# Performance work log

Hardware: AMD Instinct MI355X
Metric: run time of the kernel (lower is better)

The kernel has to match this reference:

```python
import jax, jax.numpy as jnp
import numpy as np

B, T, D, HD = 8, 2048, 768, 64

def setup_inputs() -> dict:
    key = jax.random.key(0)
    k1, k2, k3, k4 = jax.random.split(key, 4)
    scale = 1.0 / np.sqrt(D)
    return {
        "x": jax.random.normal(k1, (B, T, D), dtype=jnp.float32),
        "Wq": jax.random.normal(k2, (D, HD), dtype=jnp.float32) * scale,
        "Wk": jax.random.normal(k3, (D, HD), dtype=jnp.float32) * scale,
        "Wv": jax.random.normal(k4, (D, HD), dtype=jnp.float32) * scale,
    }

def reference(x, Wq, Wk, Wv):
    # q,k,v: [B,T,HD]
    q = jnp.einsum('btd,dh->bth', x, Wq)
    k = jnp.einsum('btd,dh->bth', x, Wk)
    v = jnp.einsum('btd,dh->bth', x, Wv)
    dk = q.shape[-1]
    # scores: [B,T,T], scaled then causally masked with -inf
    scores = jnp.einsum('bqh,bkh->bqk', q, k) / jnp.sqrt(jnp.float32(dk))
    Tq = scores.shape[-1]
    causal = jnp.tril(jnp.ones((Tq, Tq), dtype=bool))
    scores = jnp.where(causal, scores, -jnp.inf)
    attn = jax.nn.softmax(scores, axis=-1)  # dropout rate 0 (eval mode)
    return jnp.einsum('bqk,bkh->bqh', attn, v)
```

## Files before the change

### kernel.cpp

```cpp
#include <hip/hip_runtime.h>
#include <hip/hip_bf16.h>
#include <stdint.h>

#define B_  8
#define T_  2048
#define D_  768
#define HD_ 64
#define M_  (B_ * T_)

typedef short s16x8 __attribute__((ext_vector_type(8)));
typedef float f32x4 __attribute__((ext_vector_type(4)));
typedef float f32x16 __attribute__((ext_vector_type(16)));
typedef unsigned int u32;

union Frag { uint4 u; s16x8 h; };

__device__ __forceinline__ unsigned short f2bf(float f) {
    unsigned u = __builtin_bit_cast(unsigned, f);
    u += 0x7FFFu + ((u >> 16) & 1u);
    return (unsigned short)(u >> 16);
}
__device__ __forceinline__ unsigned pack_bf16x2(float lo, float hi) {
    return (unsigned)f2bf(lo) | ((unsigned)f2bf(hi) << 16);
}
__device__ __forceinline__ unsigned cvt_pk(float lo, float hi) {
    unsigned r;
    asm("v_cvt_pk_bf16_f32 %0, %1, %2" : "=v"(r) : "v"(lo), "v"(hi));
    return r;
}

__device__ __forceinline__ void gl_lds16(const void* g, void* l) {
    __builtin_amdgcn_global_load_lds(
        (const __attribute__((address_space(1))) u32*)g,
        (__attribute__((address_space(3))) u32*)l, 16, 0, 0);
}

__global__ __launch_bounds__(64) void prep_pk(const float* __restrict__ Wq,
                                              const float* __restrict__ Wk,
                                              const float* __restrict__ Wv,
                                              unsigned short* __restrict__ pk) {
    int nb = blockIdx.x / 24, kk = blockIdx.x % 24;
    int lane = threadIdx.x, g = lane >> 4, t = lane & 15;
    int mat = nb >> 2, col = (nb & 3) * 16 + t;
    const float* W = (mat == 0) ? Wq : (mat == 1) ? Wk : Wv;
    float s = (mat == 0) ? 0.18033688011112042f : 1.0f;
    float v[8];
#pragma unroll
    for (int e = 0; e < 8; e++)
        v[e] = W[(size_t)(kk * 32 + g * 8 + e) * HD_ + col] * s;
    uint4 u;
    u.x = pack_bf16x2(v[0], v[1]);
    u.y = pack_bf16x2(v[2], v[3]);
    u.z = pack_bf16x2(v[4], v[5]);
    u.w = pack_bf16x2(v[6], v[7]);
    *(uint4*)(pk + ((size_t)blockIdx.x * 64 + lane) * 8) = u;
}

__global__ __launch_bounds__(256, 2) void qkv_proj(const float* __restrict__ x,
                                                   const unsigned short* __restrict__ pk,
                                                   unsigned short* __restrict__ qo,
                                                   unsigned short* __restrict__ ko,
                                                   unsigned short* __restrict__ vt) {
    __shared__ char xs[4][8192];

    int tid = threadIdx.x, w = tid >> 6, lane = tid & 63;
    int g = lane >> 4, t = lane & 15;
    int m0 = blockIdx.x * 32;

    auto STAGE = [&](int jb) {
        int buf = jb & 3;
#pragma unroll
        for (int h = 0; h < 2; h++) {
            int s = tid + h * 256;
            int row = s >> 4;
            int a = (s & 15) ^ (row & 15);
            gl_lds16(x + (size_t)(m0 + row) * D_ + jb * 64 + a * 4,
                     &xs[buf][(w * 64 + h * 256) * 16]);
        }
    };

    const unsigned short* wp = pk + (size_t)w * 36864;
    auto LOADB = [&](Frag (&bb)[6], int jb) {
#pragma unroll
        for (int j = 0; j < 3; j++)
#pragma unroll
            for (int c = 0; c < 2; c++)
                bb[j * 2 + c].u = *(const uint4*)(wp + ((size_t)(j * 24 + jb * 2 + c) * 64 + lane) * 8);
    };

    f32x4 acc[3][2];
#pragma unroll
    for (int j = 0; j < 3; j++)
#pragma unroll
        for (int mf = 0; mf < 2; mf++) acc[j][mf] = (f32x4){0.f, 0.f, 0.f, 0.f};

    Frag bfr[3][6];
    LOADB(bfr[0], 0);
    LOADB(bfr[1], 1);
    STAGE(0); STAGE(1); STAGE(2);

#pragma unroll
    for (int jb = 0; jb < 12; jb++) {
        if (jb + 2 < 12) LOADB(bfr[(jb + 2) % 3], jb + 2);
        if (jb == 0)       asm volatile("s_waitcnt vmcnt(10)" ::: "memory");
        else if (jb == 10) asm volatile("s_waitcnt vmcnt(8)"  ::: "memory");
        else if (jb == 11) asm volatile("s_waitcnt vmcnt(0)"  ::: "memory");
        else               asm volatile("s_waitcnt vmcnt(16)" ::: "memory");
        __builtin_amdgcn_s_barrier();
        if (jb + 3 < 12) STAGE(jb + 3);
        int buf = jb & 3;

        Frag af[2][2];
#pragma unroll
        for (int mf = 0; mf < 2; mf++) {
            int r32 = mf * 16 + t;
#pragma unroll
            for (int c = 0; c < 2; c++) {
                float4 f0 = *(const float4*)(&xs[buf][r32 * 256 + (((c * 8 + g * 2 + 0) ^ t) * 16)]);
                float4 f1 = *(const float4*)(&xs[buf][r32 * 256 + (((c * 8 + g * 2 + 1) ^ t) * 16)]);
                af[mf][c].u.x = cvt_pk(f0.x, f0.y);
                af[mf][c].u.y = cvt_pk(f0.z, f0.w);
                af[mf][c].u.z = cvt_pk(f1.x, f1.y);
                af[mf][c].u.w = cvt_pk(f1.z, f1.w);
            }
        }
        __builtin_amdgcn_s_setprio(1);
#pragma unroll
        for (int j = 0; j < 3; j++)
#pragma unroll
            for (int c = 0; c < 2; c++) {
                acc[j][0] = __builtin_amdgcn_mfma_f32_16x16x32_bf16(af[0][c].h, bfr[jb % 3][j * 2 + c].h, acc[j][0], 0, 0, 0);
                acc[j][1] = __builtin_amdgcn_mfma_f32_16x16x32_bf16(af[1][c].h, bfr[jb % 3][j * 2 + c].h, acc[j][1], 0, 0, 0);
            }
        __builtin_amdgcn_s_setprio(0);
    }

#pragma unroll
    for (int j = 0; j < 3; j++) {
        int nb = w * 3 + j;
        int col = (nb & 3) * 16 + t;
#pragma unroll
        for (int mf = 0; mf < 2; mf++) {
            int row0 = m0 + mf * 16;
            if (nb < 8) {
                unsigned short* dst = (nb < 4) ? qo : ko;
#pragma unroll
                for (int r = 0; r < 4; r++)
                    dst[(size_t)(row0 + g * 4 + r) * HD_ + col] = f2bf(acc[j][mf][r]);
            } else {
                int bb = m0 >> 11;
                int trow = (row0 & 2047) + g * 4;
                uint2 pkk;
                pkk.x = cvt_pk(acc[j][mf][0], acc[j][mf][1]);
                pkk.y = cvt_pk(acc[j][mf][2], acc[j][mf][3]);
                *(uint2*)(vt + (((size_t)(bb * HD_ + col)) << 11) + trow) = pkk;
            }
        }
    }
}

__global__ __launch_bounds__(256) void attn(const unsigned short* __restrict__ qw,
                                            const unsigned short* __restrict__ kw,
                                            const unsigned short* __restrict__ vt,
                                            float* __restrict__ out) {
    __shared__ char smem[65536];

    int tid = threadIdx.x, wv = tid >> 6, lane = tid & 63;
    int hi = lane >> 5, l31 = lane & 31;
    int blk = blockIdx.x;
    int b = blk & 7, idx = blk >> 3;
    int qblk = (idx < 32) ? (63 - idx) : (idx - 32);
    int q0 = qblk * 32;
    int qg = q0 + l31;
    size_t bbase = (size_t)b * T_;
    int nt = qblk + 1;
    int ks = wv;
    int mt = (nt > ks) ? ((nt - ks + 3) >> 2) : 0;

    const unsigned short* kp = kw + bbase * HD_;
    const unsigned short* vp = vt + ((size_t)(b * HD_) << 11);
    char* KV = smem + wv * 16384;

    Frag qf[4];
#pragma unroll
    for (int c = 0; c < 4; c++)
        qf[c].u = *(const uint4*)(qw + (bbase + qg) * HD_ + c * 16 + hi * 8);

    auto STAGE = [&](int j, int buf) {
        int jj = (j < nt) ? j : (nt - 1);
        int kv0 = jj * 32;
#pragma unroll
        for (int q = 0; q < 4; q++) {
            int kr = q * 8 + (lane >> 3);
            int ka = (lane & 7) ^ (kr & 7);
            gl_lds16(kp + (size_t)(kv0 + kr) * HD_ + ka * 8, KV + buf * 4096 + q * 1024);
        }
#pragma unroll
        for (int q = 0; q < 4; q++) {
            int vd = q * 16 + (lane >> 2);
            int va = (lane & 3) ^ (vd & 3) ^ ((vd >> 2) & 3);
            gl_lds16(vp + ((size_t)vd << 11) + kv0 + va * 8, KV + 8192 + buf * 4096 + q * 1024);
        }
    };

    f32x16 o0, o1;
#pragma unroll
    for (int r = 0; r < 16; r++) { o0[r] = 0.f; o1[r] = 0.f; }
    float lacc = 0.f;

    auto QK = [&](const char* KB, f32x16& st) {
#pragma unroll
        for (int r = 0; r < 16; r++) st[r] = 0.f;
        __builtin_amdgcn_s_setprio(1);
#pragma unroll
        for (int c = 0; c < 4; c++) {
            Frag ka;
            ka.u = *(const uint4*)(KB + l31 * 128 + (((c * 2 + hi) ^ (l31 & 7)) * 16));
            st = __builtin_amdgcn_mfma_f32_32x32x16_bf16(ka.h, qf[c].h, st, 0, 0, 0);
        }
        __builtin_amdgcn_s_setprio(0);
    };

    auto SMPV = [&](f32x16& st, int j, const char* VB) {
        int kv0 = j * 32;
        if (j == qblk) {
#pragma unroll
            for (int r = 0; r < 16; r++) {
                int key = kv0 + (r & 3) + 8 * (r >> 2) + 4 * hi;
                if (key > qg) st[r] = -1e30f;
            }
        }
        float p[16], ss = 0.f;
#pragma unroll
        for (int r = 0; r < 16; r++) { p[r] = exp2f(st[r]); ss += p[r]; }
        lacc += ss;

        u32 A0 = cvt_pk(p[0], p[1]),   A1 = cvt_pk(p[2], p[3]);
        u32 B0 = cvt_pk(p[4], p[5]),   B1 = cvt_pk(p[6], p[7]);
        u32 C0 = cvt_pk(p[8], p[9]),   C1 = cvt_pk(p[10], p[11]);
        u32 D0 = cvt_pk(p[12], p[13]), D1 = cvt_pk(p[14], p[15]);
        u32 A0x = (u32)__shfl_xor((int)A0, 32);
        u32 A1x = (u32)__shfl_xor((int)A1, 32);
        u32 B0x = (u32)__shfl_xor((int)B0, 32);
        u32 B1x = (u32)__shfl_xor((int)B1, 32);
        u32 C0x = (u32)__shfl_xor((int)C0, 32);
        u32 C1x = (u32)__shfl_xor((int)C1, 32);
        u32 D0x = (u32)__shfl_xor((int)D0, 32);
        u32 D1x = (u32)__shfl_xor((int)D1, 32);
        Frag pf0, pf1;
        pf0.u.x = hi ? B0x : A0;
        pf0.u.y = hi ? B1x : A1;
        pf0.u.z = hi ? B0  : A0x;
        pf0.u.w = hi ? B1  : A1x;
        pf1.u.x = hi ? D0x : C0;
        pf1.u.y = hi ? D1x : C1;
        pf1.u.z = hi ? D0  : C0x;
        pf1.u.w = hi ? D1  : C1x;

        __builtin_amdgcn_s_setprio(1);
        {
            int sw0 = (l31 & 3) ^ ((l31 >> 2) & 3);
            Frag va;
            va.u = *(const uint4*)(VB + l31 * 64 + (((hi) ^ sw0) * 16));
            o0 = __builtin_amdgcn_mfma_f32_32x32x16_bf16(va.h, pf0.h, o0, 0, 0, 0);
            va.u = *(const uint4*)(VB + l31 * 64 + (((2 + hi) ^ sw0) * 16));
            o0 = __builtin_amdgcn_mfma_f32_32x32x16_bf16(va.h, pf1.h, o0, 0, 0, 0);
            int d1 = 32 + l31;
            int sw1 = (d1 & 3) ^ ((d1 >> 2) & 3);
            va.u = *(const uint4*)(VB + d1 * 64 + (((hi) ^ sw1) * 16));
            o1 = __builtin_amdgcn_mfma_f32_32x32x16_bf16(va.h, pf0.h, o1, 0, 0, 0);
            va.u = *(const uint4*)(VB + d1 * 64 + (((2 + hi) ^ sw1) * 16));
            o1 = __builtin_amdgcn_mfma_f32_32x32x16_bf16(va.h, pf1.h, o1, 0, 0, 0);
        }
        __builtin_amdgcn_s_setprio(0);
    };

    if (mt > 0) STAGE(ks, 0);
    if (mt > 1) STAGE(ks + 4, 1);

    int i = 0;
#pragma unroll 1
    for (; i + 2 <= mt; i += 2) {
        int ja = ks + 4 * i, jb2 = ja + 4;
        const char* KA = KV + (i & 1) * 4096;
        const char* VA = KV + 8192 + (i & 1) * 4096;
        const char* KB2 = KV + ((i + 1) & 1) * 4096;
        const char* VB2 = KV + 8192 + ((i + 1) & 1) * 4096;

        asm volatile("s_waitcnt vmcnt(12)" ::: "memory");
        f32x16 sa;
        QK(KA, sa);
        asm volatile("s_waitcnt vmcnt(4)" ::: "memory");
        f32x16 sb;
        QK(KB2, sb);
        SMPV(sa, ja, VA);
        asm volatile("s_waitcnt vmcnt(0)" ::: "memory");
        if (i + 2 < mt) STAGE(ks + 4 * (i + 2), i & 1);
        SMPV(sb, jb2, VB2);
        if (i + 3 < mt) STAGE(ks + 4 * (i + 3), (i + 1) & 1);
    }
    if (i < mt) {
        int ja = ks + 4 * i;
        const char* KA = KV + (i & 1) * 4096;
        const char* VA = KV + 8192 + (i & 1) * 4096;
        asm volatile("s_waitcnt vmcnt(4)" ::: "memory");
        f32x16 sa;
        QK(KA, sa);
        asm volatile("s_waitcnt vmcnt(0)" ::: "memory");
        SMPV(sa, ja, VA);
    }

    asm volatile("s_waitcnt vmcnt(0)" ::: "memory");
    lacc += __shfl_xor(lacc, 32);
    __syncthreads();

    float* MO = (float*)smem;
    {
        int base = (wv * 64 + lane) * 36;
#pragma unroll
        for (int qd = 0; qd < 4; qd++) {
            float4 w4;
            w4.x = o0[qd * 4 + 0]; w4.y = o0[qd * 4 + 1];
            w4.z = o0[qd * 4 + 2]; w4.w = o0[qd * 4 + 3];
            *(float4*)&MO[base + qd * 4] = w4;
            float4 v4;
            v4.x = o1[qd * 4 + 0]; v4.y = o1[qd * 4 + 1];
            v4.z = o1[qd * 4 + 2]; v4.w = o1[qd * 4 + 3];
            *(float4*)&MO[base + 16 + qd * 4] = v4;
        }
        MO[base + 32] = lacc;
    }
    __syncthreads();
    {
        int row = tid >> 3;
        int c0 = (tid & 7) * 8;
        int j0 = 4 * ((c0 & 31) >> 3) + ((c0 >> 5) << 4);
        float lsum = 0.f;
#pragma unroll
        for (int k = 0; k < 4; k++) lsum += MO[(k * 64 + row) * 36 + 32];
        float inv = 1.0f / lsum;
        float4 aq = {0.f, 0.f, 0.f, 0.f};
        float4 bq = {0.f, 0.f, 0.f, 0.f};
#pragma unroll
        for (int k = 0; k < 4; k++) {
            float4 v0 = *(const float4*)&MO[(k * 64 + row) * 36 + j0];
            float4 v1 = *(const float4*)&MO[(k * 64 + row + 32) * 36 + j0];
            aq.x += v0.x; aq.y += v0.y; aq.z += v0.z; aq.w += v0.w;
            bq.x += v1.x; bq.y += v1.y; bq.z += v1.z; bq.w += v1.w;
        }
        aq.x *= inv; aq.y *= inv; aq.z *= inv; aq.w *= inv;
        bq.x *= inv; bq.y *= inv; bq.z *= inv; bq.w *= inv;
        float* op = out + (bbase + q0 + row) * HD_ + c0;
        *(float4*)&op[0] = aq;
        *(float4*)&op[4] = bq;
    }
}

extern "C" void kernel_launch(void* const* d_in, const int* in_sizes, int n_in,
                              void* d_out, int out_size, void* d_ws, size_t ws_size,
                              hipStream_t stream) {
    const float* x  = (const float*)d_in[0];
    const float* Wq = (const float*)d_in[1];
    const float* Wk = (const float*)d_in[2];
    const float* Wv = (const float*)d_in[3];
    char* ws = (char*)d_ws;
    unsigned short* pkw = (unsigned short*)ws;
    unsigned short* qw = (unsigned short*)(ws + 294912);
    unsigned short* kw = (unsigned short*)(ws + 294912 + 2097152);
    unsigned short* vt = (unsigned short*)(ws + 294912 + 4194304);
    float* out = (float*)d_out;

    hipLaunchKernelGGL(prep_pk, dim3(288), dim3(64), 0, stream, Wq, Wk, Wv, pkw);
    hipLaunchKernelGGL(qkv_proj, dim3(M_ / 32), dim3(256), 0, stream, x, pkw, qw, kw, vt);
    hipLaunchKernelGGL(attn, dim3(512), dim3(256), 0, stream, qw, kw, vt, out);
}
```

Baseline: 41.99 us.

## Fuse weight packing, QKV projection and attention into one persistent kernel

Merges the three launches (weight pack, QKV projection, causal attention) into a single kernel of 512 blocks. The phases are separated by software grid barriers built on an atomic counter in the workspace, which is zeroed by a memset before each launch. The goal is to remove launch gaps and the tail drain between kernels. In exchange it adds a memset, two global spin barriers, and a deadlock risk unless all 512 blocks are resident at once. Using launch bounds of 2 blocks per SM with 64KB of LDS also means the attention phase runs at the occupancy set for the projection.

```diff
diff --git a/kernel.cpp b/kernel.cpp
--- a/kernel.cpp
+++ b/kernel.cpp
@@ -7,6 +7,7 @@
 #define D_  768
 #define HD_ 64
 #define M_  (B_ * T_)
+#define NBLK 512
 
 typedef short s16x8 __attribute__((ext_vector_type(8)));
 typedef float f32x4 __attribute__((ext_vector_type(4)));
@@ -35,324 +36,343 @@
         (__attribute__((address_space(3))) u32*)l, 16, 0, 0);
 }
 
-__global__ __launch_bounds__(64) void prep_pk(const float* __restrict__ Wq,
-                                              const float* __restrict__ Wk,
-                                              const float* __restrict__ Wv,
-                                              unsigned short* __restrict__ pk) {
-    int nb = blockIdx.x / 24, kk = blockIdx.x % 24;
-    int lane = threadIdx.x, g = lane >> 4, t = lane & 15;
-    int mat = nb >> 2, col = (nb & 3) * 16 + t;
-    const float* W = (mat == 0) ? Wq : (mat == 1) ? Wk : Wv;
-    float s = (mat == 0) ? 0.18033688011112042f : 1.0f;
-    float v[8];
-#pragma unroll
-    for (int e = 0; e < 8; e++)
-        v[e] = W[(size_t)(kk * 32 + g * 8 + e) * HD_ + col] * s;
-    uint4 u;
-    u.x = pack_bf16x2(v[0], v[1]);
-    u.y = pack_bf16x2(v[2], v[3]);
-    u.z = pack_bf16x2(v[4], v[5]);
-    u.w = pack_bf16x2(v[6], v[7]);
-    *(uint4*)(pk + ((size_t)blockIdx.x * 64 + lane) * 8) = u;
-}
-
-__global__ __launch_bounds__(256, 2) void qkv_proj(const float* __restrict__ x,
-                                                   const unsigned short* __restrict__ pk,
-                                                   unsigned short* __restrict__ qo,
-                                                   unsigned short* __restrict__ ko,
-                                                   unsigned short* __restrict__ vt) {
-    __shared__ char xs[4][8192];
-
-    int tid = threadIdx.x, w = tid >> 6, lane = tid & 63;
-    int g = lane >> 4, t = lane & 15;
-    int m0 = blockIdx.x * 32;
-
-    auto STAGE = [&](int jb) {
-        int buf = jb & 3;
-#pragma unroll
-        for (int h = 0; h < 2; h++) {
-            int s = tid + h * 256;
-            int row = s >> 4;
-            int a = (s & 15) ^ (row & 15);
-            gl_lds16(x + (size_t)(m0 + row) * D_ + jb * 64 + a * 4,
-                     &xs[buf][(w * 64 + h * 256) * 16]);
-        }
-    };
-
-    const unsigned short* wp = pk + (size_t)w * 36864;
-    auto LOADB = [&](Frag (&bb)[6], int jb) {
-#pragma unroll
-        for (int j = 0; j < 3; j++)
-#pragma unroll
-            for (int c = 0; c < 2; c++)
-                bb[j * 2 + c].u = *(const uint4*)(wp + ((size_t)(j * 24 + jb * 2 + c) * 64 + lane) * 8);
-    };
-
-    f32x4 acc[3][2];
-#pragma unroll
-    for (int j = 0; j < 3; j++)
-#pragma unroll
-        for (int mf = 0; mf < 2; mf++) acc[j][mf] = (f32x4){0.f, 0.f, 0.f, 0.f};
-
-    Frag bfr[3][6];
-    LOADB(bfr[0], 0);
-    LOADB(bfr[1], 1);
-    STAGE(0); STAGE(1); STAGE(2);
-
-#pragma unroll
-    for (int jb = 0; jb < 12; jb++) {
-        if (jb + 2 < 12) LOADB(bfr[(jb + 2) % 3], jb + 2);
-        if (jb == 0)       asm volatile("s_waitcnt vmcnt(10)" ::: "memory");
-        else if (jb == 10) asm volatile("s_waitcnt vmcnt(8)"  ::: "memory");
-        else if (jb == 11) asm volatile("s_waitcnt vmcnt(0)"  ::: "memory");
-        else               asm volatile("s_waitcnt vmcnt(16)" ::: "memory");
-        __builtin_amdgcn_s_barrier();
-        if (jb + 3 < 12) STAGE(jb + 3);
-        int buf = jb & 3;
-
-        Frag af[2][2];
-#pragma unroll
-        for (int mf = 0; mf < 2; mf++) {
-            int r32 = mf * 16 + t;
-#pragma unroll
-            for (int c = 0; c < 2; c++) {
-                float4 f0 = *(const float4*)(&xs[buf][r32 * 256 + (((c * 8 + g * 2 + 0) ^ t) * 16)]);
-                float4 f1 = *(const float4*)(&xs[buf][r32 * 256 + (((c * 8 + g * 2 + 1) ^ t) * 16)]);
-                af[mf][c].u.x = cvt_pk(f0.x, f0.y);
-                af[mf][c].u.y = cvt_pk(f0.z, f0.w);
-                af[mf][c].u.z = cvt_pk(f1.x, f1.y);
-                af[mf][c].u.w = cvt_pk(f1.z, f1.w);
-            }
-        }
-        __builtin_amdgcn_s_setprio(1);
-#pragma unroll
-        for (int j = 0; j < 3; j++)
-#pragma unroll
-            for (int c = 0; c < 2; c++) {
-                acc[j][0] = __builtin_amdgcn_mfma_f32_16x16x32_bf16(af[0][c].h, bfr[jb % 3][j * 2 + c].h, acc[j][0], 0, 0, 0);
-                acc[j][1] = __builtin_amdgcn_mfma_f32_16x16x32_bf16(af[1][c].h, bfr[jb % 3][j * 2 + c].h, acc[j][1], 0, 0, 0);
-            }
-        __builtin_amdgcn_s_setprio(0);
-    }
-
-#pragma unroll
-    for (int j = 0; j < 3; j++) {
-        int nb = w * 3 + j;
-        int col = (nb & 3) * 16 + t;
-#pragma unroll
-        for (int mf = 0; mf < 2; mf++) {
-            int row0 = m0 + mf * 16;
-            if (nb < 8) {
-                unsigned short* dst = (nb < 4) ? qo : ko;
-#pragma unroll
-                for (int r = 0; r < 4; r++)
-                    dst[(size_t)(row0 + g * 4 + r) * HD_ + col] = f2bf(acc[j][mf][r]);
-            } else {
-                int bb = m0 >> 11;
-                int trow = (row0 & 2047) + g * 4;
-                uint2 pkk;
-                pkk.x = cvt_pk(acc[j][mf][0], acc[j][mf][1]);
-                pkk.y = cvt_pk(acc[j][mf][2], acc[j][mf][3]);
-                *(uint2*)(vt + (((size_t)(bb * HD_ + col)) << 11) + trow) = pkk;
-            }
-        }
-    }
-}
-
-__global__ __launch_bounds__(256) void attn(const unsigned short* __restrict__ qw,
-                                            const unsigned short* __restrict__ kw,
-                                            const unsigned short* __restrict__ vt,
-                                            float* __restrict__ out) {
-    __shared__ char smem[65536];
-
-    int tid = threadIdx.x, wv = tid >> 6, lane = tid & 63;
-    int hi = lane >> 5, l31 = lane & 31;
-    int blk = blockIdx.x;
-    int b = blk & 7, idx = blk >> 3;
-    int qblk = (idx < 32) ? (63 - idx) : (idx - 32);
-    int q0 = qblk * 32;
-    int qg = q0 + l31;
-    size_t bbase = (size_t)b * T_;
-    int nt = qblk + 1;
-    int ks = wv;
-    int mt = (nt > ks) ? ((nt - ks + 3) >> 2) : 0;
-
-    const unsigned short* kp = kw + bbase * HD_;
-    const unsigned short* vp = vt + ((size_t)(b * HD_) << 11);
-    char* KV = smem + wv * 16384;
-
-    Frag qf[4];
-#pragma unroll
-    for (int c = 0; c < 4; c++)
-        qf[c].u = *(const uint4*)(qw + (bbase + qg) * HD_ + c * 16 + hi * 8);
-
-    auto STAGE = [&](int j, int buf) {
-        int jj = (j < nt) ? j : (nt - 1);
-        int kv0 = jj * 32;
-#pragma unroll
-        for (int q = 0; q < 4; q++) {
-            int kr = q * 8 + (lane >> 3);
-            int ka = (lane & 7) ^ (kr & 7);
-            gl_lds16(kp + (size_t)(kv0 + kr) * HD_ + ka * 8, KV + buf * 4096 + q * 1024);
-        }
-#pragma unroll
-        for (int q = 0; q < 4; q++) {
-            int vd = q * 16 + (lane >> 2);
-            int va = (lane & 3) ^ (vd & 3) ^ ((vd >> 2) & 3);
-            gl_lds16(vp + ((size_t)vd << 11) + kv0 + va * 8, KV + 8192 + buf * 4096 + q * 1024);
-        }
-    };
-
-    f32x16 o0, o1;
-#pragma unroll
-    for (int r = 0; r < 16; r++) { o0[r] = 0.f; o1[r] = 0.f; }
-    float lacc = 0.f;
-
-    auto QK = [&](const char* KB, f32x16& st) {
-#pragma unroll
-        for (int r = 0; r < 16; r++) st[r] = 0.f;
-        __builtin_amdgcn_s_setprio(1);
-#pragma unroll
-        for (int c = 0; c < 4; c++) {
-            Frag ka;
-            ka.u = *(const uint4*)(KB + l31 * 128 + (((c * 2 + hi) ^ (l31 & 7)) * 16));
-            st = __builtin_amdgcn_mfma_f32_32x32x16_bf16(ka.h, qf[c].h, st, 0, 0, 0);
-        }
-        __builtin_amdgcn_s_setprio(0);
-    };
-
-    auto SMPV = [&](f32x16& st, int j, const char* VB) {
-        int kv0 = j * 32;
-        if (j == qblk) {
-#pragma unroll
-            for (int r = 0; r < 16; r++) {
-                int key = kv0 + (r & 3) + 8 * (r >> 2) + 4 * hi;
-                if (key > qg) st[r] = -1e30f;
-            }
-        }
-        float p[16], ss = 0.f;
-#pragma unroll
-        for (int r = 0; r < 16; r++) { p[r] = exp2f(st[r]); ss += p[r]; }
-        lacc += ss;
-
-        u32 A0 = cvt_pk(p[0], p[1]),   A1 = cvt_pk(p[2], p[3]);
-        u32 B0 = cvt_pk(p[4], p[5]),   B1 = cvt_pk(p[6], p[7]);
-        u32 C0 = cvt_pk(p[8], p[9]),   C1 = cvt_pk(p[10], p[11]);
-        u32 D0 = cvt_pk(p[12], p[13]), D1 = cvt_pk(p[14], p[15]);
-        u32 A0x = (u32)__shfl_xor((int)A0, 32);
-        u32 A1x = (u32)__shfl_xor((int)A1, 32);
-        u32 B0x = (u32)__shfl_xor((int)B0, 32);
-        u32 B1x = (u32)__shfl_xor((int)B1, 32);
-        u32 C0x = (u32)__shfl_xor((int)C0, 32);
-        u32 C1x = (u32)__shfl_xor((int)C1, 32);
-        u32 D0x = (u32)__shfl_xor((int)D0, 32);
-        u32 D1x = (u32)__shfl_xor((int)D1, 32);
-        Frag pf0, pf1;
-        pf0.u.x = hi ? B0x : A0;
-        pf0.u.y = hi ? B1x : A1;
-        pf0.u.z = hi ? B0  : A0x;
-        pf0.u.w = hi ? B1  : A1x;
-        pf1.u.x = hi ? D0x : C0;
-        pf1.u.y = hi ? D1x : C1;
-        pf1.u.z = hi ? D0  : C0x;
-        pf1.u.w = hi ? D1  : C1x;
-
-        __builtin_amdgcn_s_setprio(1);
-        {
-            int sw0 = (l31 & 3) ^ ((l31 >> 2) & 3);
-            Frag va;
-            va.u = *(const uint4*)(VB + l31 * 64 + (((hi) ^ sw0) * 16));
-            o0 = __builtin_amdgcn_mfma_f32_32x32x16_bf16(va.h, pf0.h, o0, 0, 0, 0);
-            va.u = *(const uint4*)(VB + l31 * 64 + (((2 + hi) ^ sw0) * 16));
-            o0 = __builtin_amdgcn_mfma_f32_32x32x16_bf16(va.h, pf1.h, o0, 0, 0, 0);
-            int d1 = 32 + l31;
-            int sw1 = (d1 & 3) ^ ((d1 >> 2) & 3);
-            va.u = *(const uint4*)(VB + d1 * 64 + (((hi) ^ sw1) * 16));
-            o1 = __builtin_amdgcn_mfma_f32_32x32x16_bf16(va.h, pf0.h, o1, 0, 0, 0);
-            va.u = *(const uint4*)(VB + d1 * 64 + (((2 + hi) ^ sw1) * 16));
-            o1 = __builtin_amdgcn_mfma_f32_32x32x16_bf16(va.h, pf1.h, o1, 0, 0, 0);
-        }
-        __builtin_amdgcn_s_setprio(0);
-    };
-
-    if (mt > 0) STAGE(ks, 0);
-    if (mt > 1) STAGE(ks + 4, 1);
-
-    int i = 0;
-#pragma unroll 1
-    for (; i + 2 <= mt; i += 2) {
-        int ja = ks + 4 * i, jb2 = ja + 4;
-        const char* KA = KV + (i & 1) * 4096;
-        const char* VA = KV + 8192 + (i & 1) * 4096;
-        const char* KB2 = KV + ((i + 1) & 1) * 4096;
-        const char* VB2 = KV + 8192 + ((i + 1) & 1) * 4096;
-
-        asm volatile("s_waitcnt vmcnt(12)" ::: "memory");
-        f32x16 sa;
-        QK(KA, sa);
-        asm volatile("s_waitcnt vmcnt(4)" ::: "memory");
-        f32x16 sb;
-        QK(KB2, sb);
-        SMPV(sa, ja, VA);
-        asm volatile("s_waitcnt vmcnt(0)" ::: "memory");
-        if (i + 2 < mt) STAGE(ks + 4 * (i + 2), i & 1);
-        SMPV(sb, jb2, VB2);
-        if (i + 3 < mt) STAGE(ks + 4 * (i + 3), (i + 1) & 1);
-    }
-    if (i < mt) {
-        int ja = ks + 4 * i;
-        const char* KA = KV + (i & 1) * 4096;
-        const char* VA = KV + 8192 + (i & 1) * 4096;
-        asm volatile("s_waitcnt vmcnt(4)" ::: "memory");
-        f32x16 sa;
-        QK(KA, sa);
-        asm volatile("s_waitcnt vmcnt(0)" ::: "memory");
-        SMPV(sa, ja, VA);
-    }
-
-    asm volatile("s_waitcnt vmcnt(0)" ::: "memory");
-    lacc += __shfl_xor(lacc, 32);
+__device__ __forceinline__ void grid_barrier(unsigned* cnt) {
     __syncthreads();
-
-    float* MO = (float*)smem;
-    {
-        int base = (wv * 64 + lane) * 36;
-#pragma unroll
-        for (int qd = 0; qd < 4; qd++) {
-            float4 w4;
-            w4.x = o0[qd * 4 + 0]; w4.y = o0[qd * 4 + 1];
-            w4.z = o0[qd * 4 + 2]; w4.w = o0[qd * 4 + 3];
-            *(float4*)&MO[base + qd * 4] = w4;
-            float4 v4;
-            v4.x = o1[qd * 4 + 0]; v4.y = o1[qd * 4 + 1];
-            v4.z = o1[qd * 4 + 2]; v4.w = o1[qd * 4 + 3];
-            *(float4*)&MO[base + 16 + qd * 4] = v4;
-        }
-        MO[base + 32] = lacc;
+    if (threadIdx.x == 0) {
+        __threadfence();
+        __hip_atomic_fetch_add(cnt, 1u, __ATOMIC_ACQ_REL, __HIP_MEMORY_SCOPE_AGENT);
+        while (__hip_atomic_load(cnt, __ATOMIC_ACQUIRE, __HIP_MEMORY_SCOPE_AGENT) < (unsigned)NBLK)
+            __builtin_amdgcn_s_sleep(2);
+        __threadfence();
     }
     __syncthreads();
+}
+
+__global__ __launch_bounds__(256, 2) void fused(const float* __restrict__ x,
+                                                const float* __restrict__ Wq,
+                                                const float* __restrict__ Wk,
+                                                const float* __restrict__ Wv,
+                                                unsigned short* __restrict__ pk,
+                                                unsigned short* __restrict__ qo,
+                                                unsigned short* __restrict__ ko,
+                                                unsigned short* __restrict__ vt,
+                                                float* __restrict__ out,
+                                                unsigned* __restrict__ cnt) {
+    __shared__ char smem[65536];
+    int tid = threadIdx.x, blk = blockIdx.x;
+
     {
-        int row = tid >> 3;
-        int c0 = (tid & 7) * 8;
-        int j0 = 4 * ((c0 & 31) >> 3) + ((c0 >> 5) << 4);
-        float lsum = 0.f;
-#pragma unroll
-        for (int k = 0; k < 4; k++) lsum += MO[(k * 64 + row) * 36 + 32];
-        float inv = 1.0f / lsum;
-        float4 aq = {0.f, 0.f, 0.f, 0.f};
-        float4 bq = {0.f, 0.f, 0.f, 0.f};
-#pragma unroll
-        for (int k = 0; k < 4; k++) {
-            float4 v0 = *(const float4*)&MO[(k * 64 + row) * 36 + j0];
-            float4 v1 = *(const float4*)&MO[(k * 64 + row + 32) * 36 + j0];
-            aq.x += v0.x; aq.y += v0.y; aq.z += v0.z; aq.w += v0.w;
-            bq.x += v1.x; bq.y += v1.y; bq.z += v1.z; bq.w += v1.w;
-        }
-        aq.x *= inv; aq.y *= inv; aq.z *= inv; aq.w *= inv;
-        bq.x *= inv; bq.y *= inv; bq.z *= inv; bq.w *= inv;
-        float* op = out + (bbase + q0 + row) * HD_ + c0;
-        *(float4*)&op[0] = aq;
-        *(float4*)&op[4] = bq;
+        int id = blk * 256 + tid;
+        if (id < 288 * 64) {
+            int tile = id >> 6, lane = id & 63;
+            int nb = tile / 24, kk = tile % 24;
+            int g = lane >> 4, t = lane & 15;
+            int mat = nb >> 2, col = (nb & 3) * 16 + t;
+            const float* W = (mat == 0) ? Wq : (mat == 1) ? Wk : Wv;
+            float s = (mat == 0) ? 0.18033688011112042f : 1.0f;
+            float v[8];
+#pragma unroll
+            for (int e = 0; e < 8; e++)
+                v[e] = W[(size_t)(kk * 32 + g * 8 + e) * HD_ + col] * s;
+            uint4 u;
+            u.x = pack_bf16x2(v[0], v[1]);
+            u.y = pack_bf16x2(v[2], v[3]);
+            u.z = pack_bf16x2(v[4], v[5]);
+            u.w = pack_bf16x2(v[6], v[7]);
+            *(uint4*)(pk + ((size_t)tile * 64 + lane) * 8) = u;
+        }
+    }
+    grid_barrier(cnt);
+
+    {
+        char (*xs)[8192] = (char(*)[8192])smem;
+
+        int w = tid >> 6, lane = tid & 63;
+        int g = lane >> 4, t = lane & 15;
+        int m0 = blk * 32;
+
+        auto STAGE = [&](int jb) {
+            int buf = jb & 3;
+#pragma unroll
+            for (int h = 0; h < 2; h++) {
+                int s = tid + h * 256;
+                int row = s >> 4;
+                int a = (s & 15) ^ (row & 15);
+                gl_lds16(x + (size_t)(m0 + row) * D_ + jb * 64 + a * 4,
+                         &xs[buf][(w * 64 + h * 256) * 16]);
+            }
+        };
+
+        const unsigned short* wp = pk + (size_t)w * 36864;
+        auto LOADB = [&](Frag (&bb)[6], int jb) {
+#pragma unroll
+            for (int j = 0; j < 3; j++)
+#pragma unroll
+                for (int c = 0; c < 2; c++)
+                    bb[j * 2 + c].u = *(const uint4*)(wp + ((size_t)(j * 24 + jb * 2 + c) * 64 + lane) * 8);
+        };
+
+        f32x4 acc[3][2];
+#pragma unroll
+        for (int j = 0; j < 3; j++)
+#pragma unroll
+            for (int mf = 0; mf < 2; mf++) acc[j][mf] = (f32x4){0.f, 0.f, 0.f, 0.f};
+
+        Frag bfr[3][6];
+        LOADB(bfr[0], 0);
+        LOADB(bfr[1], 1);
+        STAGE(0); STAGE(1); STAGE(2);
+
+#pragma unroll
+        for (int jb = 0; jb < 12; jb++) {
+            if (jb + 2 < 12) LOADB(bfr[(jb + 2) % 3], jb + 2);
+            if (jb == 0)       asm volatile("s_waitcnt vmcnt(10)" ::: "memory");
+            else if (jb == 10) asm volatile("s_waitcnt vmcnt(8)"  ::: "memory");
+            else if (jb == 11) asm volatile("s_waitcnt vmcnt(0)"  ::: "memory");
+            else               asm volatile("s_waitcnt vmcnt(16)" ::: "memory");
+            __builtin_amdgcn_s_barrier();
+            if (jb + 3 < 12) STAGE(jb + 3);
+            int buf = jb & 3;
+
+            Frag af[2][2];
+#pragma unroll
+            for (int mf = 0; mf < 2; mf++) {
+                int r32 = mf * 16 + t;
+#pragma unroll
+                for (int c = 0; c < 2; c++) {
+                    float4 f0 = *(const float4*)(&xs[buf][r32 * 256 + (((c * 8 + g * 2 + 0) ^ t) * 16)]);
+                    float4 f1 = *(const float4*)(&xs[buf][r32 * 256 + (((c * 8 + g * 2 + 1) ^ t) * 16)]);
+                    af[mf][c].u.x = cvt_pk(f0.x, f0.y);
+                    af[mf][c].u.y = cvt_pk(f0.z, f0.w);
+                    af[mf][c].u.z = cvt_pk(f1.x, f1.y);
+                    af[mf][c].u.w = cvt_pk(f1.z, f1.w);
+                }
+            }
+            __builtin_amdgcn_s_setprio(1);
+#pragma unroll
+            for (int j = 0; j < 3; j++)
+#pragma unroll
+                for (int c = 0; c < 2; c++) {
+                    acc[j][0] = __builtin_amdgcn_mfma_f32_16x16x32_bf16(af[0][c].h, bfr[jb % 3][j * 2 + c].h, acc[j][0], 0, 0, 0);
+                    acc[j][1] = __builtin_amdgcn_mfma_f32_16x16x32_bf16(af[1][c].h, bfr[jb % 3][j * 2 + c].h, acc[j][1], 0, 0, 0);
+                }
+            __builtin_amdgcn_s_setprio(0);
+        }
+
+#pragma unroll
+        for (int j = 0; j < 3; j++) {
+            int nb = w * 3 + j;
+            int col = (nb & 3) * 16 + t;
+#pragma unroll
+            for (int mf = 0; mf < 2; mf++) {
+                int row0 = m0 + mf * 16;
+                if (nb < 8) {
+                    unsigned short* dst = (nb < 4) ? qo : ko;
+#pragma unroll
+                    for (int r = 0; r < 4; r++)
+                        dst[(size_t)(row0 + g * 4 + r) * HD_ + col] = f2bf(acc[j][mf][r]);
+                } else {
+                    int bb = m0 >> 11;
+                    int trow = (row0 & 2047) + g * 4;
+                    uint2 pkk;
+                    pkk.x = cvt_pk(acc[j][mf][0], acc[j][mf][1]);
+                    pkk.y = cvt_pk(acc[j][mf][2], acc[j][mf][3]);
+                    *(uint2*)(vt + (((size_t)(bb * HD_ + col)) << 11) + trow) = pkk;
+                }
+            }
+        }
+    }
+    grid_barrier(cnt + 16);
+
+    {
+        int wv = tid >> 6, lane = tid & 63;
+        int hi = lane >> 5, l31 = lane & 31;
+        int b = blk & 7, idx = blk >> 3;
+        int qblk = (idx < 32) ? (63 - idx) : (idx - 32);
+        int q0 = qblk * 32;
+        int qg = q0 + l31;
+        size_t bbase = (size_t)b * T_;
+        int nt = qblk + 1;
+        int ks = wv;
+        int mt = (nt > ks) ? ((nt - ks + 3) >> 2) : 0;
+
+        const unsigned short* kp = ko + bbase * HD_;
+        const unsigned short* vp = vt + ((size_t)(b * HD_) << 11);
+        char* KV = smem + wv * 16384;
+
+        Frag qf[4];
+#pragma unroll
+        for (int c = 0; c < 4; c++)
+            qf[c].u = *(const uint4*)(qo + (bbase + qg) * HD_ + c * 16 + hi * 8);
+
+        auto STAGE = [&](int j, int buf) {
+            int jj = (j < nt) ? j : (nt - 1);
+            int kv0 = jj * 32;
+#pragma unroll
+            for (int q = 0; q < 4; q++) {
+                int kr = q * 8 + (lane >> 3);
+                int ka = (lane & 7) ^ (kr & 7);
+                gl_lds16(kp + (size_t)(kv0 + kr) * HD_ + ka * 8, KV + buf * 4096 + q * 1024);
+            }
+#pragma unroll
+            for (int q = 0; q < 4; q++) {
+                int vd = q * 16 + (lane >> 2);
+                int va = (lane & 3) ^ (vd & 3) ^ ((vd >> 2) & 3);
+                gl_lds16(vp + ((size_t)vd << 11) + kv0 + va * 8, KV + 8192 + buf * 4096 + q * 1024);
+            }
+        };
+
+        f32x16 o0, o1;
+#pragma unroll
+        for (int r = 0; r < 16; r++) { o0[r] = 0.f; o1[r] = 0.f; }
+        float lacc = 0.f;
+
+        auto QK = [&](const char* KB, f32x16& st) {
+#pragma unroll
+            for (int r = 0; r < 16; r++) st[r] = 0.f;
+            __builtin_amdgcn_s_setprio(1);
+#pragma unroll
+            for (int c = 0; c < 4; c++) {
+                Frag ka;
+                ka.u = *(const uint4*)(KB + l31 * 128 + (((c * 2 + hi) ^ (l31 & 7)) * 16));
+                st = __builtin_amdgcn_mfma_f32_32x32x16_bf16(ka.h, qf[c].h, st, 0, 0, 0);
+            }
+            __builtin_amdgcn_s_setprio(0);
+        };
+
+        auto SMPV = [&](f32x16& st, int j, const char* VB) {
+            int kv0 = j * 32;
+            if (j == qblk) {
+#pragma unroll
+                for (int r = 0; r < 16; r++) {
+                    int key = kv0 + (r & 3) + 8 * (r >> 2) + 4 * hi;
+                    if (key > qg) st[r] = -1e30f;
+                }
+            }
+            float p[16], ss = 0.f;
+#pragma unroll
+            for (int r = 0; r < 16; r++) { p[r] = exp2f(st[r]); ss += p[r]; }
+            lacc += ss;
+
+            u32 A0 = cvt_pk(p[0], p[1]),   A1 = cvt_pk(p[2], p[3]);
+            u32 B0 = cvt_pk(p[4], p[5]),   B1 = cvt_pk(p[6], p[7]);
+            u32 C0 = cvt_pk(p[8], p[9]),   C1 = cvt_pk(p[10], p[11]);
+            u32 D0 = cvt_pk(p[12], p[13]), D1 = cvt_pk(p[14], p[15]);
+            u32 A0x = (u32)__shfl_xor((int)A0, 32);
+            u32 A1x = (u32)__shfl_xor((int)A1, 32);
+            u32 B0x = (u32)__shfl_xor((int)B0, 32);
+            u32 B1x = (u32)__shfl_xor((int)B1, 32);
+            u32 C0x = (u32)__shfl_xor((int)C0, 32);
+            u32 C1x = (u32)__shfl_xor((int)C1, 32);
+            u32 D0x = (u32)__shfl_xor((int)D0, 32);
+            u32 D1x = (u32)__shfl_xor((int)D1, 32);
+            Frag pf0, pf1;
+            pf0.u.x = hi ? B0x : A0;
+            pf0.u.y = hi ? B1x : A1;
+            pf0.u.z = hi ? B0  : A0x;
+            pf0.u.w = hi ? B1  : A1x;
+            pf1.u.x = hi ? D0x : C0;
+            pf1.u.y = hi ? D1x : C1;
+            pf1.u.z = hi ? D0  : C0x;
+            pf1.u.w = hi ? D1  : C1x;
+
+            __builtin_amdgcn_s_setprio(1);
+            {
+                int sw0 = (l31 & 3) ^ ((l31 >> 2) & 3);
+                Frag va;
+                va.u = *(const uint4*)(VB + l31 * 64 + (((hi) ^ sw0) * 16));
+                o0 = __builtin_amdgcn_mfma_f32_32x32x16_bf16(va.h, pf0.h, o0, 0, 0, 0);
+                va.u = *(const uint4*)(VB + l31 * 64 + (((2 + hi) ^ sw0) * 16));
+                o0 = __builtin_amdgcn_mfma_f32_32x32x16_bf16(va.h, pf1.h, o0, 0, 0, 0);
+                int d1 = 32 + l31;
+                int sw1 = (d1 & 3) ^ ((d1 >> 2) & 3);
+                va.u = *(const uint4*)(VB + d1 * 64 + (((hi) ^ sw1) * 16));
+                o1 = __builtin_amdgcn_mfma_f32_32x32x16_bf16(va.h, pf0.h, o1, 0, 0, 0);
+                va.u = *(const uint4*)(VB + d1 * 64 + (((2 + hi) ^ sw1) * 16));
+                o1 = __builtin_amdgcn_mfma_f32_32x32x16_bf16(va.h, pf1.h, o1, 0, 0, 0);
+            }
+            __builtin_amdgcn_s_setprio(0);
+        };
+
+        if (mt > 0) STAGE(ks, 0);
+        if (mt > 1) STAGE(ks + 4, 1);
+
+        int i = 0;
+#pragma unroll 1
+        for (; i + 2 <= mt; i += 2) {
+            int ja = ks + 4 * i, jb2 = ja + 4;
+            const char* KA = KV + (i & 1) * 4096;
+            const char* VA = KV + 8192 + (i & 1) * 4096;
+            const char* KB2 = KV + ((i + 1) & 1) * 4096;
+            const char* VB2 = KV + 8192 + ((i + 1) & 1) * 4096;
+
+            asm volatile("s_waitcnt vmcnt(12)" ::: "memory");
+            f32x16 sa;
+            QK(KA, sa);
+            asm volatile("s_waitcnt vmcnt(4)" ::: "memory");
+            f32x16 sb;
+            QK(KB2, sb);
+            SMPV(sa, ja, VA);
+            asm volatile("s_waitcnt vmcnt(0)" ::: "memory");
+            if (i + 2 < mt) STAGE(ks + 4 * (i + 2), i & 1);
+            SMPV(sb, jb2, VB2);
+            if (i + 3 < mt) STAGE(ks + 4 * (i + 3), (i + 1) & 1);
+        }
+        if (i < mt) {
+            int ja = ks + 4 * i;
+            const char* KA = KV + (i & 1) * 4096;
+            const char* VA = KV + 8192 + (i & 1) * 4096;
+            asm volatile("s_waitcnt vmcnt(4)" ::: "memory");
+            f32x16 sa;
+            QK(KA, sa);
+            asm volatile("s_waitcnt vmcnt(0)" ::: "memory");
+            SMPV(sa, ja, VA);
+        }
+
+        asm volatile("s_waitcnt vmcnt(0)" ::: "memory");
+        lacc += __shfl_xor(lacc, 32);
+        __syncthreads();
+
+        float* MO = (float*)smem;
+        {
+            int base = (wv * 64 + lane) * 36;
+#pragma unroll
+            for (int qd = 0; qd < 4; qd++) {
+                float4 w4;
+                w4.x = o0[qd * 4 + 0]; w4.y = o0[qd * 4 + 1];
+                w4.z = o0[qd * 4 + 2]; w4.w = o0[qd * 4 + 3];
+                *(float4*)&MO[base + qd * 4] = w4;
+                float4 v4;
+                v4.x = o1[qd * 4 + 0]; v4.y = o1[qd * 4 + 1];
+                v4.z = o1[qd * 4 + 2]; v4.w = o1[qd * 4 + 3];
+                *(float4*)&MO[base + 16 + qd * 4] = v4;
+            }
+            MO[base + 32] = lacc;
+        }
+        __syncthreads();
+        {
+            int row = tid >> 3;
+            int c0 = (tid & 7) * 8;
+            int j0 = 4 * ((c0 & 31) >> 3) + ((c0 >> 5) << 4);
+            float lsum = 0.f;
+#pragma unroll
+            for (int k = 0; k < 4; k++) lsum += MO[(k * 64 + row) * 36 + 32];
+            float inv = 1.0f / lsum;
+            float4 aq = {0.f, 0.f, 0.f, 0.f};
+            float4 bq = {0.f, 0.f, 0.f, 0.f};
+#pragma unroll
+            for (int k = 0; k < 4; k++) {
+                float4 v0 = *(const float4*)&MO[(k * 64 + row) * 36 + j0];
+                float4 v1 = *(const float4*)&MO[(k * 64 + row + 32) * 36 + j0];
+                aq.x += v0.x; aq.y += v0.y; aq.z += v0.z; aq.w += v0.w;
+                bq.x += v1.x; bq.y += v1.y; bq.z += v1.z; bq.w += v1.w;
+            }
+            aq.x *= inv; aq.y *= inv; aq.z *= inv; aq.w *= inv;
+            bq.x *= inv; bq.y *= inv; bq.z *= inv; bq.w *= inv;
+            float* op = out + (bbase + q0 + row) * HD_ + c0;
+            *(float4*)&op[0] = aq;
+            *(float4*)&op[4] = bq;
+        }
     }
 }
 
@@ -368,9 +388,10 @@
     unsigned short* qw = (unsigned short*)(ws + 294912);
     unsigned short* kw = (unsigned short*)(ws + 294912 + 2097152);
     unsigned short* vt = (unsigned short*)(ws + 294912 + 4194304);
+    unsigned* cnt = (unsigned*)(ws + 294912 + 6291456);
     float* out = (float*)d_out;
 
-    hipLaunchKernelGGL(prep_pk, dim3(288), dim3(64), 0, stream, Wq, Wk, Wv, pkw);
-    hipLaunchKernelGGL(qkv_proj, dim3(M_ / 32), dim3(256), 0, stream, x, pkw, qw, kw, vt);
-    hipLaunchKernelGGL(attn, dim3(512), dim3(256), 0, stream, qw, kw, vt, out);
-}
+    hipMemsetAsync(cnt, 0, 128, stream);
+    hipLaunchKernelGGL(fused, dim3(NBLK), dim3(256), 0, stream,
+                       x, Wq, Wk, Wv, pkw, qw, kw, vt, out, cnt);
+}
```

After: 157.8 us. 3.76x slower.

## Fuse weight packing into projection kernel with global atomic counter handoff

Applied to the files above, without the earlier changes.

Removes the separate prep_pk launch by having the first 72 blocks of qkv_proj pack the bf16 weight fragments, then signal completion through an agent-scope atomic counter. All blocks issue their x staging loads first, spin-wait on the counter, then load the packed weights. The waitcnt values are adjusted for the reordered loads. This saves a kernel launch and its gap but adds a memset, a grid-wide spin dependency that needs the producer blocks to be resident, and extra latency for blocks waiting on the packing.

```diff
diff --git a/kernel.cpp b/kernel.cpp
--- a/kernel.cpp
+++ b/kernel.cpp
@@ -35,37 +35,45 @@
         (__attribute__((address_space(3))) u32*)l, 16, 0, 0);
 }
 
-__global__ __launch_bounds__(64) void prep_pk(const float* __restrict__ Wq,
-                                              const float* __restrict__ Wk,
-                                              const float* __restrict__ Wv,
-                                              unsigned short* __restrict__ pk) {
-    int nb = blockIdx.x / 24, kk = blockIdx.x % 24;
-    int lane = threadIdx.x, g = lane >> 4, t = lane & 15;
-    int mat = nb >> 2, col = (nb & 3) * 16 + t;
-    const float* W = (mat == 0) ? Wq : (mat == 1) ? Wk : Wv;
-    float s = (mat == 0) ? 0.18033688011112042f : 1.0f;
-    float v[8];
-#pragma unroll
-    for (int e = 0; e < 8; e++)
-        v[e] = W[(size_t)(kk * 32 + g * 8 + e) * HD_ + col] * s;
-    uint4 u;
-    u.x = pack_bf16x2(v[0], v[1]);
-    u.y = pack_bf16x2(v[2], v[3]);
-    u.z = pack_bf16x2(v[4], v[5]);
-    u.w = pack_bf16x2(v[6], v[7]);
-    *(uint4*)(pk + ((size_t)blockIdx.x * 64 + lane) * 8) = u;
-}
-
 __global__ __launch_bounds__(256, 2) void qkv_proj(const float* __restrict__ x,
-                                                   const unsigned short* __restrict__ pk,
+                                                   const float* __restrict__ Wq,
+                                                   const float* __restrict__ Wk,
+                                                   const float* __restrict__ Wv,
+                                                   unsigned short* __restrict__ pk,
                                                    unsigned short* __restrict__ qo,
                                                    unsigned short* __restrict__ ko,
-                                                   unsigned short* __restrict__ vt) {
+                                                   unsigned short* __restrict__ vt,
+                                                   unsigned* __restrict__ cnt) {
     __shared__ char xs[4][8192];
 
     int tid = threadIdx.x, w = tid >> 6, lane = tid & 63;
     int g = lane >> 4, t = lane & 15;
-    int m0 = blockIdx.x * 32;
+    int blk = blockIdx.x;
+    int m0 = blk * 32;
+
+    if (blk < 72) {
+        int id = blk * 256 + tid;
+        int tile = id >> 6, plane = id & 63;
+        int nb = tile / 24, kk = tile % 24;
+        int pg = plane >> 4, pt = plane & 15;
+        int mat = nb >> 2, col = (nb & 3) * 16 + pt;
+        const float* W = (mat == 0) ? Wq : (mat == 1) ? Wk : Wv;
+        float s = (mat == 0) ? 0.18033688011112042f : 1.0f;
+        float v[8];
+#pragma unroll
+        for (int e = 0; e < 8; e++)
+            v[e] = W[(size_t)(kk * 32 + pg * 8 + e) * HD_ + col] * s;
+        uint4 u;
+        u.x = pack_bf16x2(v[0], v[1]);
+        u.y = pack_bf16x2(v[2], v[3]);
+        u.z = pack_bf16x2(v[4], v[5]);
+        u.w = pack_bf16x2(v[6], v[7]);
+        *(uint4*)(pk + ((size_t)tile * 64 + plane) * 8) = u;
+        __threadfence();
+        __syncthreads();
+        if (tid == 0)
+            __hip_atomic_fetch_add(cnt, 1u, __ATOMIC_RELAXED, __HIP_MEMORY_SCOPE_AGENT);
+    }
 
     auto STAGE = [&](int jb) {
         int buf = jb & 3;
@@ -79,6 +87,15 @@
         }
     };
 
+    STAGE(0); STAGE(1); STAGE(2);
+
+    if (tid == 0) {
+        while (__hip_atomic_load(cnt, __ATOMIC_RELAXED, __HIP_MEMORY_SCOPE_AGENT) < 72u)
+            __builtin_amdgcn_s_sleep(4);
+        __threadfence();
+    }
+    __syncthreads();
+
     const unsigned short* wp = pk + (size_t)w * 36864;
     auto LOADB = [&](Frag (&bb)[6], int jb) {
 #pragma unroll
@@ -97,12 +114,12 @@
     Frag bfr[3][6];
     LOADB(bfr[0], 0);
     LOADB(bfr[1], 1);
-    STAGE(0); STAGE(1); STAGE(2);
 
 #pragma unroll
     for (int jb = 0; jb < 12; jb++) {
         if (jb + 2 < 12) LOADB(bfr[(jb + 2) % 3], jb + 2);
-        if (jb == 0)       asm volatile("s_waitcnt vmcnt(10)" ::: "memory");
+        if (jb == 0)       asm volatile("s_waitcnt vmcnt(12)" ::: "memory");
+        else if (jb == 1)  asm volatile("s_waitcnt vmcnt(14)" ::: "memory");
         else if (jb == 10) asm volatile("s_waitcnt vmcnt(8)"  ::: "memory");
         else if (jb == 11) asm volatile("s_waitcnt vmcnt(0)"  ::: "memory");
         else               asm volatile("s_waitcnt vmcnt(16)" ::: "memory");
@@ -368,9 +385,11 @@
     unsigned short* qw = (unsigned short*)(ws + 294912);
     unsigned short* kw = (unsigned short*)(ws + 294912 + 2097152);
     unsigned short* vt = (unsigned short*)(ws + 294912 + 4194304);
+    unsigned* cnt = (unsigned*)(ws + 294912 + 6291456);
     float* out = (float*)d_out;
 
-    hipLaunchKernelGGL(prep_pk, dim3(288), dim3(64), 0, stream, Wq, Wk, Wv, pkw);
-    hipLaunchKernelGGL(qkv_proj, dim3(M_ / 32), dim3(256), 0, stream, x, pkw, qw, kw, vt);
+    hipMemsetAsync(cnt, 0, 64, stream);
+    hipLaunchKernelGGL(qkv_proj, dim3(M_ / 32), dim3(256), 0, stream,
+                       x, Wq, Wk, Wv, pkw, qw, kw, vt, cnt);
     hipLaunchKernelGGL(attn, dim3(512), dim3(256), 0, stream, qw, kw, vt, out);
 }
```

Result: slower. 63.22 us (+50.6%).
